# Performance work log

Hardware: AMD Instinct MI355X
Metric: run time of the kernel (lower is better)

## Reference

```python
import jax, jax.numpy as jnp
import numpy as np

LOG_CLAMP = -100.0  # torch BCE clamps log terms at -100


def _weights_from_target(target):
    # target: [B, 1, W, W]; weight[b,i,j] = W / (sqrt((i-x)^2 + (j-y)^2) + 1)
    # where (x, y) is the mean location of the per-sample max of target.
    B = target.shape[0]
    W = target.shape[-1]
    t = target.reshape(B, W, W)
    m = jnp.max(t, axis=(1, 2), keepdims=True)
    mask = (t == m).astype(t.dtype)                      # all argmax locations
    cnt = jnp.sum(mask, axis=(1, 2))                     # [B]
    idx = jnp.arange(W, dtype=t.dtype)
    x = jnp.sum(mask * idx[None, :, None], axis=(1, 2)) / cnt  # mean row index
    y = jnp.sum(mask * idx[None, None, :], axis=(1, 2)) / cnt  # mean col index
    a = idx[None, :, None] - x[:, None, None]            # [B, W, 1]
    b = idx[None, None, :] - y[:, None, None]            # [B, 1, W]
    dist = (jnp.sqrt(a * a + b * b) + 1.0) / W           # [B, W, W]
    return (1.0 / dist).reshape(target.shape)


def reference(input, target):
    weights = _weights_from_target(target)
    log_p = jnp.maximum(jnp.log(input), LOG_CLAMP)
    log_1mp = jnp.maximum(jnp.log1p(-input), LOG_CLAMP)
    bce = -(target * log_p + (1.0 - target) * log_1mp)
    return jnp.mean(weights * bce)


def setup_inputs() -> dict:
    key = jax.random.key(0)
    k1, k2 = jax.random.split(key)
    shape = (256, 1, 224, 224)
    # BCE requires probabilities in (0,1); keep strictly inside via small margin.
    input = jax.random.uniform(k1, shape, dtype=jnp.float32, minval=1e-4, maxval=1.0 - 1e-4)
    target = jax.random.uniform(k2, shape, dtype=jnp.float32)
    return {"input": input, "target": target}
```

## Files before the change

### kernel.cpp

```cpp
#include <hip/hip_runtime.h>
#include <hip/hip_fp16.h>
#include <math.h>


#define WIMG 224
#define WW (WIMG * WIMG)
#define NQ (WW / 4)
#define NB 256
#define NT 1024
#define NIT (NQ / NT)
#define REM (NQ - NIT * NT)
#define LDS_BYTES (2 * NQ * 4)
#define LN2 0.69314718055994530942f
#define CLAMP2 (-144.269504088896340736f)

__device__ __forceinline__ void stat_upd(float val, float fi, float fj,
                                         float& m, float& cnt, float& si, float& sj)
{
    bool gt = val > m;
    bool eq = val == m;
    cnt = gt ? 1.0f : (cnt + (eq ? 1.0f : 0.0f));
    si  = gt ? fi   : (si  + (eq ? fi   : 0.0f));
    sj  = gt ? fj   : (sj  + (eq ? fj   : 0.0f));
    m   = fmaxf(m, val);
}

__device__ __forceinline__ float bce2_elem(float p, float t)
{
    float lp2  = fmaxf(__builtin_amdgcn_logf(p),        CLAMP2);
    float l1p2 = fmaxf(__builtin_amdgcn_logf(1.0f - p), CLAMP2);
    return l1p2 + t * (lp2 - l1p2);
}

__global__ __launch_bounds__(NT, 4) void floss_kernel(
    const float* __restrict__ input,
    const float* __restrict__ target,
    float* __restrict__ out,
    float inv_total)
{
    extern __shared__ __half2 bce_lds[];
    const int b   = blockIdx.x;
    const int tid = threadIdx.x;
    const float4* __restrict__ t4 = (const float4*)(target + (size_t)b * WW);
    const float4* __restrict__ p4 = (const float4*)(input  + (size_t)b * WW);

    float m = -1.0f, cnt = 0.0f, si = 0.0f, sj = 0.0f;
    #pragma unroll 4
    for (int it = 0; it < NIT; ++it) {
        int q = it * NT + tid;
        float4 tv = t4[q];
        float4 pv = p4[q];
        int i  = q / 56;
        int j0 = (q - i * 56) * 4;
        float fi = (float)i;
        stat_upd(tv.x, fi, (float)(j0 + 0), m, cnt, si, sj);
        stat_upd(tv.y, fi, (float)(j0 + 1), m, cnt, si, sj);
        stat_upd(tv.z, fi, (float)(j0 + 2), m, cnt, si, sj);
        stat_upd(tv.w, fi, (float)(j0 + 3), m, cnt, si, sj);
        float b0 = bce2_elem(pv.x, tv.x);
        float b1 = bce2_elem(pv.y, tv.y);
        float b2 = bce2_elem(pv.z, tv.z);
        float b3 = bce2_elem(pv.w, tv.w);
        bce_lds[q]      = __floats2half2_rn(b0, b1);
        bce_lds[NQ + q] = __floats2half2_rn(b2, b3);
    }
    const bool has_tail = tid < REM;
    const int qt = NIT * NT + tid;
    if (has_tail) {
        float4 tv = t4[qt];
        float4 pv = p4[qt];
        int i  = qt / 56;
        int j0 = (qt - i * 56) * 4;
        float fi = (float)i;
        stat_upd(tv.x, fi, (float)(j0 + 0), m, cnt, si, sj);
        stat_upd(tv.y, fi, (float)(j0 + 1), m, cnt, si, sj);
        stat_upd(tv.z, fi, (float)(j0 + 2), m, cnt, si, sj);
        stat_upd(tv.w, fi, (float)(j0 + 3), m, cnt, si, sj);
        bce_lds[qt]      = __floats2half2_rn(bce2_elem(pv.x, tv.x), bce2_elem(pv.y, tv.y));
        bce_lds[NQ + qt] = __floats2half2_rn(bce2_elem(pv.z, tv.z), bce2_elem(pv.w, tv.w));
    }

    #pragma unroll
    for (int off = 32; off > 0; off >>= 1) {
        float m2  = __shfl_down(m,   off);
        float c2  = __shfl_down(cnt, off);
        float si2 = __shfl_down(si,  off);
        float sj2 = __shfl_down(sj,  off);
        bool gt = m2 > m, eq = m2 == m;
        cnt = gt ? c2  : (cnt + (eq ? c2  : 0.0f));
        si  = gt ? si2 : (si  + (eq ? si2 : 0.0f));
        sj  = gt ? sj2 : (sj  + (eq ? sj2 : 0.0f));
        m   = fmaxf(m, m2);
    }
    __shared__ float sm[16], sc[16], ssi[16], ssj[16];
    __shared__ float sxy[2];
    const int lane = tid & 63, wid = tid >> 6;
    if (lane == 0) { sm[wid] = m; sc[wid] = cnt; ssi[wid] = si; ssj[wid] = sj; }
    __syncthreads();
    if (tid == 0) {
        float M = sm[0], C = sc[0], SI = ssi[0], SJ = ssj[0];
        #pragma unroll
        for (int w = 1; w < 16; ++w) {
            float mw = sm[w];
            bool gt = mw > M, eq = mw == M;
            C  = gt ? sc[w]  : (C  + (eq ? sc[w]  : 0.0f));
            SI = gt ? ssi[w] : (SI + (eq ? ssi[w] : 0.0f));
            SJ = gt ? ssj[w] : (SJ + (eq ? ssj[w] : 0.0f));
            M  = fmaxf(M, mw);
        }
        sxy[0] = SI / C;
        sxy[1] = SJ / C;
    }
    __syncthreads();
    const float x = sxy[0], y = sxy[1];
    const float Kc = -(float)WIMG * LN2;

    float acc = 0.0f;
    #pragma unroll
    for (int it = 0; it <= NIT; ++it) {
        if (it == NIT && !has_tail) break;
        int q = (it < NIT) ? (it * NT + tid) : qt;
        float2 b01 = __half22float2(bce_lds[q]);
        float2 b23 = __half22float2(bce_lds[NQ + q]);
        int i  = q / 56;
        int j0 = (q - i * 56) * 4;
        float di  = (float)i - x;
        float di2 = di * di;
        float bb[4] = {b01.x, b01.y, b23.x, b23.y};
        #pragma unroll
        for (int k = 0; k < 4; ++k) {
            float dj = (float)(j0 + k) - y;
            float s  = __builtin_amdgcn_sqrtf(di2 + dj * dj);
            float wf = Kc * __builtin_amdgcn_rcpf(s + 1.0f);
            acc += wf * bb[k];
        }
    }

    #pragma unroll
    for (int off = 32; off > 0; off >>= 1) acc += __shfl_down(acc, off);
    __shared__ float sred[16];
    if (lane == 0) sred[wid] = acc;
    __syncthreads();
    if (tid == 0) {
        float ssum = 0.0f;
        #pragma unroll
        for (int w = 0; w < 16; ++w) ssum += sred[w];
        atomicAdd(out, ssum * inv_total);
    }
}

extern "C" void kernel_launch(void* const* d_in, const int* in_sizes, int n_in,
                              void* d_out, int out_size, void* d_ws, size_t ws_size,
                              hipStream_t stream) {
    const float* input  = (const float*)d_in[0];
    const float* target = (const float*)d_in[1];
    float* out = (float*)d_out;
    hipFuncSetAttribute((const void*)floss_kernel,
                        hipFuncAttributeMaxDynamicSharedMemorySize, LDS_BYTES);
    hipMemsetAsync(out, 0, sizeof(float), stream);
    const float inv_total = 1.0f / (256.0f * 224.0f * 224.0f);
    floss_kernel<<<NB, NT, LDS_BYTES, stream>>>(input, target, out, inv_total);
}
```

Before: 124.9 us.

## Prefetch loads two iterations ahead and reduce argmax stats per float4

The main loop now software-pipelines global loads, issuing the loads for iteration it+2 while computing iteration it, and the tail loads are issued up front. The per-element running argmax update is replaced by a local max/count/column-sum over each float4 group, then one merge per group. The launch_bounds minimum-blocks hint is dropped. The aim is to hide memory latency with only one 1024-thread block per SM (256 blocks), at the cost of more live registers.

```diff
diff --git a/kernel.cpp b/kernel.cpp
--- a/kernel.cpp
+++ b/kernel.cpp
@@ -14,17 +14,6 @@
 #define LN2 0.69314718055994530942f
 #define CLAMP2 (-144.269504088896340736f)
 
-__device__ __forceinline__ void stat_upd(float val, float fi, float fj,
-                                         float& m, float& cnt, float& si, float& sj)
-{
-    bool gt = val > m;
-    bool eq = val == m;
-    cnt = gt ? 1.0f : (cnt + (eq ? 1.0f : 0.0f));
-    si  = gt ? fi   : (si  + (eq ? fi   : 0.0f));
-    sj  = gt ? fj   : (sj  + (eq ? fj   : 0.0f));
-    m   = fmaxf(m, val);
-}
-
 __device__ __forceinline__ float bce2_elem(float p, float t)
 {
     float lp2  = fmaxf(__builtin_amdgcn_logf(p),        CLAMP2);
@@ -32,7 +21,7 @@
     return l1p2 + t * (lp2 - l1p2);
 }
 
-__global__ __launch_bounds__(NT, 4) void floss_kernel(
+__global__ __launch_bounds__(NT) void floss_kernel(
     const float* __restrict__ input,
     const float* __restrict__ target,
     float* __restrict__ out,
@@ -44,40 +33,65 @@
     const float4* __restrict__ t4 = (const float4*)(target + (size_t)b * WW);
     const float4* __restrict__ p4 = (const float4*)(input  + (size_t)b * WW);
 
+    const bool has_tail = tid < REM;
+    const int qt = NIT * NT + tid;
+    float4 tvt = {}, pvt = {};
+    if (has_tail) { tvt = t4[qt]; pvt = p4[qt]; }
+
     float m = -1.0f, cnt = 0.0f, si = 0.0f, sj = 0.0f;
-    #pragma unroll 4
+    float4 tva = t4[tid],      pva = p4[tid];
+    float4 tvb = t4[NT + tid], pvb = p4[NT + tid];
+    #pragma unroll
     for (int it = 0; it < NIT; ++it) {
-        int q = it * NT + tid;
-        float4 tv = t4[q];
-        float4 pv = p4[q];
+        float4 tvn, pvn;
+        if (it + 2 < NIT) { tvn = t4[(it + 2) * NT + tid]; pvn = p4[(it + 2) * NT + tid]; }
+        float4 tv = tva, pv = pva;
+        int q  = it * NT + tid;
         int i  = q / 56;
         int j0 = (q - i * 56) * 4;
         float fi = (float)i;
-        stat_upd(tv.x, fi, (float)(j0 + 0), m, cnt, si, sj);
-        stat_upd(tv.y, fi, (float)(j0 + 1), m, cnt, si, sj);
-        stat_upd(tv.z, fi, (float)(j0 + 2), m, cnt, si, sj);
-        stat_upd(tv.w, fi, (float)(j0 + 3), m, cnt, si, sj);
-        float b0 = bce2_elem(pv.x, tv.x);
-        float b1 = bce2_elem(pv.y, tv.y);
-        float b2 = bce2_elem(pv.z, tv.z);
-        float b3 = bce2_elem(pv.w, tv.w);
-        bce_lds[q]      = __floats2half2_rn(b0, b1);
-        bce_lds[NQ + q] = __floats2half2_rn(b2, b3);
+
+        float mq  = fmaxf(fmaxf(tv.x, tv.y), fmaxf(tv.z, tv.w));
+        float cq  = (tv.x == mq ? 1.0f : 0.0f) + (tv.y == mq ? 1.0f : 0.0f)
+                  + (tv.z == mq ? 1.0f : 0.0f) + (tv.w == mq ? 1.0f : 0.0f);
+        float sjq = (tv.x == mq ? (float)(j0 + 0) : 0.0f)
+                  + (tv.y == mq ? (float)(j0 + 1) : 0.0f)
+                  + (tv.z == mq ? (float)(j0 + 2) : 0.0f)
+                  + (tv.w == mq ? (float)(j0 + 3) : 0.0f);
+        float siq = fi * cq;
+        bool gt = mq > m, eq = mq == m;
+        cnt = gt ? cq  : (cnt + (eq ? cq  : 0.0f));
+        si  = gt ? siq : (si  + (eq ? siq : 0.0f));
+        sj  = gt ? sjq : (sj  + (eq ? sjq : 0.0f));
+        m   = fmaxf(m, mq);
+
+        bce_lds[q]      = __floats2half2_rn(bce2_elem(pv.x, tv.x), bce2_elem(pv.y, tv.y));
+        bce_lds[NQ + q] = __floats2half2_rn(bce2_elem(pv.z, tv.z), bce2_elem(pv.w, tv.w));
+
+        tva = tvb; pva = pvb;
+        tvb = tvn; pvb = pvn;
     }
-    const bool has_tail = tid < REM;
-    const int qt = NIT * NT + tid;
     if (has_tail) {
-        float4 tv = t4[qt];
-        float4 pv = p4[qt];
-        int i  = qt / 56;
-        int j0 = (qt - i * 56) * 4;
+        int q  = qt;
+        int i  = q / 56;
+        int j0 = (q - i * 56) * 4;
         float fi = (float)i;
-        stat_upd(tv.x, fi, (float)(j0 + 0), m, cnt, si, sj);
-        stat_upd(tv.y, fi, (float)(j0 + 1), m, cnt, si, sj);
-        stat_upd(tv.z, fi, (float)(j0 + 2), m, cnt, si, sj);
-        stat_upd(tv.w, fi, (float)(j0 + 3), m, cnt, si, sj);
-        bce_lds[qt]      = __floats2half2_rn(bce2_elem(pv.x, tv.x), bce2_elem(pv.y, tv.y));
-        bce_lds[NQ + qt] = __floats2half2_rn(bce2_elem(pv.z, tv.z), bce2_elem(pv.w, tv.w));
+        float4 tv = tvt, pv = pvt;
+        float mq  = fmaxf(fmaxf(tv.x, tv.y), fmaxf(tv.z, tv.w));
+        float cq  = (tv.x == mq ? 1.0f : 0.0f) + (tv.y == mq ? 1.0f : 0.0f)
+                  + (tv.z == mq ? 1.0f : 0.0f) + (tv.w == mq ? 1.0f : 0.0f);
+        float sjq = (tv.x == mq ? (float)(j0 + 0) : 0.0f)
+                  + (tv.y == mq ? (float)(j0 + 1) : 0.0f)
+                  + (tv.z == mq ? (float)(j0 + 2) : 0.0f)
+                  + (tv.w == mq ? (float)(j0 + 3) : 0.0f);
+        float siq = fi * cq;
+        bool gt = mq > m, eq = mq == m;
+        cnt = gt ? cq  : (cnt + (eq ? cq  : 0.0f));
+        si  = gt ? siq : (si  + (eq ? siq : 0.0f));
+        sj  = gt ? sjq : (sj  + (eq ? sjq : 0.0f));
+        m   = fmaxf(m, mq);
+        bce_lds[q]      = __floats2half2_rn(bce2_elem(pv.x, tv.x), bce2_elem(pv.y, tv.y));
+        bce_lds[NQ + q] = __floats2half2_rn(bce2_elem(pv.z, tv.z), bce2_elem(pv.w, tv.w));
     }
 
     #pragma unroll
```

Measured after the change: 122.2 us. 1.02x faster.
